# Kernel optimization log

Measured on AMD Instinct MI355X. Metric: run time of the kernel, lower is better.

The kernel has to match this reference:

```python
import jax, jax.numpy as jnp
import numpy as np

DIM = 1024
HEADS = 16
DIM_HEAD = 64
INNER = HEADS * DIM_HEAD  # 1024
EPS = 1e-5


def setup_inputs() -> dict:
    key = jax.random.key(0)
    ks = jax.random.split(key, 8)
    B, N = 4, 2048
    s = 0.02
    return {
        "query": jax.random.normal(ks[0], (B, N, DIM), jnp.float32),
        "key_": jax.random.normal(ks[1], (B, N, DIM), jnp.float32),
        "value": jax.random.normal(ks[2], (B, N, DIM), jnp.float32),
        "Wq": jax.random.normal(ks[3], (DIM, INNER), jnp.float32) * s,
        "Wk": jax.random.normal(ks[4], (DIM, INNER), jnp.float32) * s,
        "Wv": jax.random.normal(ks[5], (DIM, INNER), jnp.float32) * s,
        "Wo": jax.random.normal(ks[6], (INNER, DIM), jnp.float32) * s,
        "bo": jnp.zeros((DIM,), jnp.float32),
        "gamma": jnp.ones((DIM,), jnp.float32),
        "beta": jnp.zeros((DIM,), jnp.float32),
    }


def reference(query, key_, value, Wq, Wk, Wv, Wo, bo, gamma, beta):
    B, N, _ = query.shape
    scale = DIM_HEAD ** (-0.5)
    # project and split heads: [B, H, N, Dh]
    q = (query @ Wq).reshape(B, N, HEADS, DIM_HEAD).transpose(0, 2, 1, 3)
    k = (key_ @ Wk).reshape(B, N, HEADS, DIM_HEAD).transpose(0, 2, 1, 3)
    v = (value @ Wv).reshape(B, N, HEADS, DIM_HEAD).transpose(0, 2, 1, 3)
    dots = jnp.einsum("bhnd,bhmd->bhnm", q, k) * scale  # [B,H,N,N]
    attn = jax.nn.softmax(dots, axis=-1)
    out = jnp.einsum("bhnm,bhmd->bhnd", attn, v)
    out = out.transpose(0, 2, 1, 3).reshape(B, N, INNER)
    out = out @ Wo + bo  # dropout p=0.0 is identity
    # LayerNorm over last dim
    mu = out.mean(-1, keepdims=True)
    var = ((out - mu) ** 2).mean(-1, keepdims=True)
    normed = (out - mu) * jax.lax.rsqrt(var + EPS) * gamma + beta
    return normed + query
```

## Files before the change

### kernel.cpp

```cpp
#include <hip/hip_runtime.h>
#include <stdint.h>

#define K_DIM 1024
#define B_SZ 4
#define N_SEQ 2048
#define HEADS 16
#define DH 64
#define M_TOT (B_SZ * N_SEQ)

typedef __bf16 bf16x8 __attribute__((ext_vector_type(8)));
typedef __bf16 bf16x4 __attribute__((ext_vector_type(4)));
typedef float f32x4 __attribute__((ext_vector_type(4)));

typedef const uint32_t __attribute__((address_space(1))) gas_u32;
typedef uint32_t __attribute__((address_space(3))) las_u32;

__device__ __forceinline__ uint16_t f2bf(float f) {
  uint32_t u = __float_as_uint(f);
  u += 0x7FFFu + ((u >> 16) & 1u);
  return (uint16_t)(u >> 16);
}

__device__ __forceinline__ void gld_lds16(const uint16_t* g, uint16_t* lds) {
  __builtin_amdgcn_global_load_lds((gas_u32*)g, (las_u32*)lds, 16, 0, 0);
}

__global__ __launch_bounds__(256) void conv_bf16_k(const float* __restrict__ src,
                                                   uint16_t* __restrict__ dst, int n4) {
  int i = blockIdx.x * blockDim.x + threadIdx.x;
  if (i < n4) {
    float4 v = ((const float4*)src)[i];
    ushort4 o;
    o.x = f2bf(v.x); o.y = f2bf(v.y); o.z = f2bf(v.z); o.w = f2bf(v.w);
    ((ushort4*)dst)[i] = o;
  }
}

__global__ __launch_bounds__(256) void transpose_conv(const float* __restrict__ src,
                                                      uint16_t* __restrict__ dst) {
  __shared__ float tile[32][33];
  const int tx = threadIdx.x, ty = threadIdx.y;
  const int bx = blockIdx.x * 32, by = blockIdx.y * 32;
#pragma unroll
  for (int i = 0; i < 32; i += 8)
    tile[ty + i][tx] = src[(size_t)(by + ty + i) * 1024 + bx + tx];
  __syncthreads();
#pragma unroll
  for (int i = 0; i < 32; i += 8)
    dst[(size_t)(bx + ty + i) * 1024 + by + tx] = f2bf(tile[tx][ty + i]);
}

template <int MODE>
__global__ __launch_bounds__(256, 2) void gemm_bf16(const uint16_t* __restrict__ A,
                                                    const uint16_t* __restrict__ BT,
                                                    void* __restrict__ Cout,
                                                    const float* __restrict__ bias) {
  __shared__ __align__(16) uint16_t As[128 * 32];
  __shared__ __align__(16) uint16_t Bs[128 * 32];
  const int tid = threadIdx.x;
  const int wave = tid >> 6, lane = tid & 63;
  const int g = lane >> 4, c16 = lane & 15;
  const int m0 = blockIdx.y * 128, n0 = blockIdx.x * 128;
  const int wr = wave >> 1, wc = wave & 1;

  const f32x4 fzero = {0.f, 0.f, 0.f, 0.f};
  f32x4 acc[4][4];
#pragma unroll
  for (int i = 0; i < 4; ++i)
#pragma unroll
    for (int j = 0; j < 4; ++j) acc[i][j] = fzero;

  const int srow = wave * 32 + (lane >> 2);
  const int scol = (lane & 3) * 8;
  const uint16_t* ag0 = A + (size_t)(m0 + srow) * K_DIM + scol;
  const uint16_t* ag1 = A + (size_t)(m0 + srow + 16) * K_DIM + scol;
  const uint16_t* bg0 = BT + (size_t)(n0 + srow) * K_DIM + scol;
  const uint16_t* bg1 = BT + (size_t)(n0 + srow + 16) * K_DIM + scol;
  uint16_t* la0 = &As[(wave * 32) * 32];
  uint16_t* la1 = &As[(wave * 32 + 16) * 32];
  uint16_t* lb0 = &Bs[(wave * 32) * 32];
  uint16_t* lb1 = &Bs[(wave * 32 + 16) * 32];

  for (int kt = 0; kt < K_DIM / 32; ++kt) {
    __syncthreads();
    gld_lds16(ag0 + kt * 32, la0);
    gld_lds16(ag1 + kt * 32, la1);
    gld_lds16(bg0 + kt * 32, lb0);
    gld_lds16(bg1 + kt * 32, lb1);
    __syncthreads();
    bf16x8 avec[4], bvec[4];
#pragma unroll
    for (int i = 0; i < 4; ++i)
      avec[i] = *(const bf16x8*)&As[(wr * 64 + i * 16 + c16) * 32 + g * 8];
#pragma unroll
    for (int j = 0; j < 4; ++j)
      bvec[j] = *(const bf16x8*)&Bs[(wc * 64 + j * 16 + c16) * 32 + g * 8];
#pragma unroll
    for (int i = 0; i < 4; ++i)
#pragma unroll
      for (int j = 0; j < 4; ++j)
        acc[i][j] = __builtin_amdgcn_mfma_f32_16x16x32_bf16(avec[i], bvec[j], acc[i][j], 0, 0, 0);
  }

#pragma unroll
  for (int i = 0; i < 4; ++i) {
#pragma unroll
    for (int j = 0; j < 4; ++j) {
      const int col = n0 + wc * 64 + j * 16 + c16;
      if (MODE == 2) {
        const int h = col >> 6, d = col & 63;
        const int row0 = m0 + wr * 64 + i * 16 + g * 4;
        const int b = row0 >> 11, n = row0 & 2047;
        ushort4 o;
        o.x = f2bf(acc[i][j][0]); o.y = f2bf(acc[i][j][1]);
        o.z = f2bf(acc[i][j][2]); o.w = f2bf(acc[i][j][3]);
        *(ushort4*)&((uint16_t*)Cout)[(((size_t)(b * HEADS + h)) * DH + d) * N_SEQ + n] = o;
      } else {
#pragma unroll
        for (int r = 0; r < 4; ++r) {
          const int row = m0 + wr * 64 + i * 16 + g * 4 + r;
          if (MODE == 0) {
            const int b = row >> 11, n = row & 2047;
            const int h = col >> 6, d = col & 63;
            ((uint16_t*)Cout)[(((size_t)(b * HEADS + h)) * N_SEQ + n) * DH + d] = f2bf(acc[i][j][r]);
          } else {
            ((float*)Cout)[(size_t)row * 1024 + col] = acc[i][j][r] + bias[col];
          }
        }
      }
    }
  }
}

__global__ __launch_bounds__(256, 2) void attention_k(const uint16_t* __restrict__ qm,
                                                      const uint16_t* __restrict__ km,
                                                      const uint16_t* __restrict__ vtm,
                                                      uint16_t* __restrict__ om) {
  __shared__ __align__(16) uint16_t Ks[64 * 72];
  __shared__ __align__(16) uint16_t Vs[64 * 72];
  __shared__ __align__(16) uint16_t Pt[4][64 * 88];
  const int tid = threadIdx.x;
  const int wave = tid >> 6, lane = tid & 63;
  const int g = lane >> 4, c16 = lane & 15;
  const int bh = blockIdx.y, b = bh >> 4, h = bh & 15;
  const int q0 = blockIdx.x * 256 + wave * 64;

  const uint16_t* qbase = qm + (size_t)bh * N_SEQ * DH;
  const uint16_t* kbase = km + (size_t)bh * N_SEQ * DH;
  const uint16_t* vbase = vtm + (size_t)bh * DH * N_SEQ;

  bf16x8 qf[4][2];
#pragma unroll
  for (int qc = 0; qc < 4; ++qc) {
    const uint16_t* qp = qbase + (size_t)(q0 + qc * 16 + c16) * DH + g * 8;
    qf[qc][0] = *(const bf16x8*)qp;
    qf[qc][1] = *(const bf16x8*)(qp + 32);
  }

  const f32x4 fz = {0.f, 0.f, 0.f, 0.f};
  f32x4 oacc[4][4];
#pragma unroll
  for (int qc = 0; qc < 4; ++qc)
#pragma unroll
    for (int jt = 0; jt < 4; ++jt) oacc[qc][jt] = fz;
  float l[4] = {0.f, 0.f, 0.f, 0.f};

  const float CE = 0.1803368801f;
  uint16_t* ptw = Pt[wave];

  for (int t = 0; t < N_SEQ / 64; ++t) {
    __syncthreads();
#pragma unroll
    for (int p = 0; p < 2; ++p) {
      const int e = (p * 256 + tid) * 8;
      *(uint4*)&Ks[(e >> 6) * 72 + (e & 63)] = *(const uint4*)&kbase[(size_t)t * 4096 + e];
      const int c = p * 256 + tid;
      const int vr = c >> 3, vc = (c & 7) * 8;
      *(uint4*)&Vs[vr * 72 + vc] = *(const uint4*)&vbase[(size_t)vr * N_SEQ + t * 64 + vc];
    }
    __syncthreads();

#pragma unroll
    for (int kt = 0; kt < 4; ++kt) {
      bf16x8 kf0 = *(const bf16x8*)&Ks[(kt * 16 + c16) * 72 + g * 8];
      bf16x8 kf1 = *(const bf16x8*)&Ks[(kt * 16 + c16) * 72 + 32 + g * 8];
#pragma unroll
      for (int qc = 0; qc < 4; ++qc) {
        f32x4 z = fz;
        z = __builtin_amdgcn_mfma_f32_16x16x32_bf16(kf0, qf[qc][0], z, 0, 0, 0);
        z = __builtin_amdgcn_mfma_f32_16x16x32_bf16(kf1, qf[qc][1], z, 0, 0, 0);
        const float p0 = __builtin_amdgcn_exp2f(z[0] * CE);
        const float p1 = __builtin_amdgcn_exp2f(z[1] * CE);
        const float p2 = __builtin_amdgcn_exp2f(z[2] * CE);
        const float p3 = __builtin_amdgcn_exp2f(z[3] * CE);
        l[qc] += (p0 + p1) + (p2 + p3);
        bf16x4 pk;
        pk[0] = (__bf16)p0; pk[1] = (__bf16)p1; pk[2] = (__bf16)p2; pk[3] = (__bf16)p3;
        *(bf16x4*)&ptw[(qc * 16 + c16) * 88 + kt * 16 + g * 4] = pk;
      }
    }

#pragma unroll
    for (int kc = 0; kc < 2; ++kc) {
      bf16x8 pa[4];
#pragma unroll
      for (int qc = 0; qc < 4; ++qc)
        pa[qc] = *(const bf16x8*)&ptw[(qc * 16 + c16) * 88 + kc * 32 + g * 8];
#pragma unroll
      for (int jt = 0; jt < 4; ++jt) {
        bf16x8 vb = *(const bf16x8*)&Vs[(jt * 16 + c16) * 72 + kc * 32 + g * 8];
#pragma unroll
        for (int qc = 0; qc < 4; ++qc)
          oacc[qc][jt] = __builtin_amdgcn_mfma_f32_16x16x32_bf16(pa[qc], vb, oacc[qc][jt], 0, 0, 0);
      }
    }
  }

#pragma unroll
  for (int qc = 0; qc < 4; ++qc) {
    l[qc] += __shfl_xor(l[qc], 16);
    l[qc] += __shfl_xor(l[qc], 32);
  }

#pragma unroll
  for (int qc = 0; qc < 4; ++qc) {
#pragma unroll
    for (int r = 0; r < 4; ++r) {
      const float lr = __shfl(l[qc], g * 4 + r, 16);
      const float inv = 1.f / lr;
      const int row = q0 + qc * 16 + g * 4 + r;
      const size_t base = ((size_t)b * N_SEQ + row) * 1024 + h * 64;
#pragma unroll
      for (int jt = 0; jt < 4; ++jt)
        om[base + jt * 16 + c16] = f2bf(oacc[qc][jt][r] * inv);
    }
  }
}

__global__ __launch_bounds__(256) void ln_res_k(const float* __restrict__ proj,
                                                const float* __restrict__ query,
                                                const float* __restrict__ gamma,
                                                const float* __restrict__ beta,
                                                float* __restrict__ out) {
  const int row = blockIdx.x;
  const int tid = threadIdx.x;
  const size_t base = (size_t)row * 1024 + tid * 4;
  float4 v = *(const float4*)(proj + base);
  float s = v.x + v.y + v.z + v.w;
  float s2 = v.x * v.x + v.y * v.y + v.z * v.z + v.w * v.w;
#pragma unroll
  for (int off = 1; off < 64; off <<= 1) {
    s += __shfl_xor(s, off);
    s2 += __shfl_xor(s2, off);
  }
  __shared__ float red[8];
  const int wave = tid >> 6, lane = tid & 63;
  if (lane == 0) { red[wave] = s; red[4 + wave] = s2; }
  __syncthreads();
  s = red[0] + red[1] + red[2] + red[3];
  s2 = red[4] + red[5] + red[6] + red[7];
  const float mu = s * (1.f / 1024.f);
  const float var = fmaxf(s2 * (1.f / 1024.f) - mu * mu, 0.f);
  const float rstd = rsqrtf(var + 1e-5f);
  float4 gq = *(const float4*)(gamma + tid * 4);
  float4 bq = *(const float4*)(beta + tid * 4);
  float4 qq = *(const float4*)(query + base);
  float4 o;
  o.x = (v.x - mu) * rstd * gq.x + bq.x + qq.x;
  o.y = (v.y - mu) * rstd * gq.y + bq.y + qq.y;
  o.z = (v.z - mu) * rstd * gq.z + bq.z + qq.z;
  o.w = (v.w - mu) * rstd * gq.w + bq.w + qq.w;
  *(float4*)(out + base) = o;
}

extern "C" void kernel_launch(void* const* d_in, const int* in_sizes, int n_in,
                              void* d_out, int out_size, void* d_ws, size_t ws_size,
                              hipStream_t stream) {
  (void)in_sizes; (void)n_in; (void)out_size; (void)ws_size;
  const float* query = (const float*)d_in[0];
  const float* key_ = (const float*)d_in[1];
  const float* value = (const float*)d_in[2];
  const float* Wq = (const float*)d_in[3];
  const float* Wk = (const float*)d_in[4];
  const float* Wv = (const float*)d_in[5];
  const float* Wo = (const float*)d_in[6];
  const float* bo = (const float*)d_in[7];
  const float* gamma = (const float*)d_in[8];
  const float* beta = (const float*)d_in[9];
  float* out = (float*)d_out;

  const size_t NELEM = (size_t)M_TOT * 1024;
  uint16_t* wsp = (uint16_t*)d_ws;
  uint16_t* WqT = wsp;
  uint16_t* WkT = WqT + 1024 * 1024;
  uint16_t* WvT = WkT + 1024 * 1024;
  uint16_t* WoT = WvT + 1024 * 1024;
  uint16_t* xq = WoT + 1024 * 1024;
  uint16_t* xk = xq + NELEM;
  uint16_t* xv = xk + NELEM;
  uint16_t* qb = xv + NELEM;
  uint16_t* kb = qb + NELEM;
  uint16_t* vt = kb + NELEM;
  uint16_t* attnO = xq;
  float* proj = (float*)xk;

  const int n4 = (int)(NELEM / 4);
  conv_bf16_k<<<8192, 256, 0, stream>>>(query, xq, n4);
  conv_bf16_k<<<8192, 256, 0, stream>>>(key_, xk, n4);
  conv_bf16_k<<<8192, 256, 0, stream>>>(value, xv, n4);

  dim3 tb(32, 8);
  transpose_conv<<<dim3(32, 32), tb, 0, stream>>>(Wq, WqT);
  transpose_conv<<<dim3(32, 32), tb, 0, stream>>>(Wk, WkT);
  transpose_conv<<<dim3(32, 32), tb, 0, stream>>>(Wv, WvT);
  transpose_conv<<<dim3(32, 32), tb, 0, stream>>>(Wo, WoT);

  dim3 gg(8, 64);
  gemm_bf16<0><<<gg, 256, 0, stream>>>(xq, WqT, qb, nullptr);
  gemm_bf16<0><<<gg, 256, 0, stream>>>(xk, WkT, kb, nullptr);
  gemm_bf16<2><<<gg, 256, 0, stream>>>(xv, WvT, vt, nullptr);

  attention_k<<<dim3(N_SEQ / 256, 64), 256, 0, stream>>>(qb, kb, vt, attnO);

  gemm_bf16<1><<<gg, 256, 0, stream>>>(attnO, WoT, proj, bo);

  ln_res_k<<<8192, 256, 0, stream>>>(proj, query, gamma, beta, out);
}
```

Before: 391.2 us.

## Batch launches, fold softmax scale into Q, swizzle attention LDS, shrink attention tiles

Merges the three input conversions, the four weight transposes and the Q/K projection GEMMs into single launches indexed by blockIdx.y or blockIdx.z. The softmax scale (with the log2e factor) is folded into the Q projection epilogue, which removes a multiply per score in the attention loop. Attention LDS tiles drop their padding in favour of XOR swizzling to avoid bank conflicts. Each wave now handles 32 query rows instead of 64, with launch bounds raised to 4 blocks and twice as many blocks. The trade-off is that each K/V tile loaded into LDS is reused by fewer query rows.

```diff
diff --git a/kernel.cpp b/kernel.cpp
--- a/kernel.cpp
+++ b/kernel.cpp
@@ -15,6 +15,8 @@
 typedef const uint32_t __attribute__((address_space(1))) gas_u32;
 typedef uint32_t __attribute__((address_space(3))) las_u32;
 
+#define CE_SCALE 0.1803368801f
+
 __device__ __forceinline__ uint16_t f2bf(float f) {
   uint32_t u = __float_as_uint(f);
   u += 0x7FFFu + ((u >> 16) & 1u);
@@ -25,8 +27,13 @@
   __builtin_amdgcn_global_load_lds((gas_u32*)g, (las_u32*)lds, 16, 0, 0);
 }
 
-__global__ __launch_bounds__(256) void conv_bf16_k(const float* __restrict__ src,
-                                                   uint16_t* __restrict__ dst, int n4) {
+__global__ __launch_bounds__(256) void conv_bf16_k(const float* __restrict__ s0,
+                                                   const float* __restrict__ s1,
+                                                   const float* __restrict__ s2,
+                                                   uint16_t* __restrict__ dstbase, int n4) {
+  const int z = blockIdx.y;
+  const float* src = (z == 0) ? s0 : (z == 1) ? s1 : s2;
+  uint16_t* dst = dstbase + (size_t)z * M_TOT * K_DIM;
   int i = blockIdx.x * blockDim.x + threadIdx.x;
   if (i < n4) {
     float4 v = ((const float4*)src)[i];
@@ -36,9 +43,15 @@
   }
 }
 
-__global__ __launch_bounds__(256) void transpose_conv(const float* __restrict__ src,
-                                                      uint16_t* __restrict__ dst) {
+__global__ __launch_bounds__(256) void transpose_conv(const float* __restrict__ s0,
+                                                      const float* __restrict__ s1,
+                                                      const float* __restrict__ s2,
+                                                      const float* __restrict__ s3,
+                                                      uint16_t* __restrict__ dstbase) {
   __shared__ float tile[32][33];
+  const int z = blockIdx.z;
+  const float* src = (z == 0) ? s0 : (z == 1) ? s1 : (z == 2) ? s2 : s3;
+  uint16_t* dst = dstbase + (size_t)z * 1024 * 1024;
   const int tx = threadIdx.x, ty = threadIdx.y;
   const int bx = blockIdx.x * 32, by = blockIdx.y * 32;
 #pragma unroll
@@ -62,6 +75,14 @@
   const int g = lane >> 4, c16 = lane & 15;
   const int m0 = blockIdx.y * 128, n0 = blockIdx.x * 128;
   const int wr = wave >> 1, wc = wave & 1;
+  float scale = 1.f;
+  if (MODE == 0) {
+    const int z = blockIdx.z;
+    A += (size_t)z * M_TOT * K_DIM;
+    BT += (size_t)z * 1024 * 1024;
+    Cout = (void*)((uint16_t*)Cout + (size_t)z * M_TOT * K_DIM);
+    scale = (z == 0) ? CE_SCALE : 1.f;
+  }
 
   const f32x4 fzero = {0.f, 0.f, 0.f, 0.f};
   f32x4 acc[4][4];
@@ -122,7 +143,8 @@
           if (MODE == 0) {
             const int b = row >> 11, n = row & 2047;
             const int h = col >> 6, d = col & 63;
-            ((uint16_t*)Cout)[(((size_t)(b * HEADS + h)) * N_SEQ + n) * DH + d] = f2bf(acc[i][j][r]);
+            ((uint16_t*)Cout)[(((size_t)(b * HEADS + h)) * N_SEQ + n) * DH + d] =
+                f2bf(acc[i][j][r] * scale);
           } else {
             ((float*)Cout)[(size_t)row * 1024 + col] = acc[i][j][r] + bias[col];
           }
@@ -132,98 +154,106 @@
   }
 }
 
-__global__ __launch_bounds__(256, 2) void attention_k(const uint16_t* __restrict__ qm,
+__global__ __launch_bounds__(256, 4) void attention_k(const uint16_t* __restrict__ qm,
                                                       const uint16_t* __restrict__ km,
                                                       const uint16_t* __restrict__ vtm,
                                                       uint16_t* __restrict__ om) {
-  __shared__ __align__(16) uint16_t Ks[64 * 72];
-  __shared__ __align__(16) uint16_t Vs[64 * 72];
-  __shared__ __align__(16) uint16_t Pt[4][64 * 88];
+  __shared__ __align__(16) uint16_t Ks[64 * 64];
+  __shared__ __align__(16) uint16_t Vs[64 * 64];
+  __shared__ __align__(16) uint16_t Pt[4][32 * 64];
   const int tid = threadIdx.x;
   const int wave = tid >> 6, lane = tid & 63;
   const int g = lane >> 4, c16 = lane & 15;
   const int bh = blockIdx.y, b = bh >> 4, h = bh & 15;
-  const int q0 = blockIdx.x * 256 + wave * 64;
+  const int q0 = blockIdx.x * 128 + wave * 32;
 
   const uint16_t* qbase = qm + (size_t)bh * N_SEQ * DH;
   const uint16_t* kbase = km + (size_t)bh * N_SEQ * DH;
   const uint16_t* vbase = vtm + (size_t)bh * DH * N_SEQ;
 
-  bf16x8 qf[4][2];
-#pragma unroll
-  for (int qc = 0; qc < 4; ++qc) {
+  bf16x8 qf[2][2];
+#pragma unroll
+  for (int qc = 0; qc < 2; ++qc) {
     const uint16_t* qp = qbase + (size_t)(q0 + qc * 16 + c16) * DH + g * 8;
     qf[qc][0] = *(const bf16x8*)qp;
     qf[qc][1] = *(const bf16x8*)(qp + 32);
   }
 
   const f32x4 fz = {0.f, 0.f, 0.f, 0.f};
-  f32x4 oacc[4][4];
-#pragma unroll
-  for (int qc = 0; qc < 4; ++qc)
+  f32x4 oacc[2][4];
+#pragma unroll
+  for (int qc = 0; qc < 2; ++qc)
 #pragma unroll
     for (int jt = 0; jt < 4; ++jt) oacc[qc][jt] = fz;
-  float l[4] = {0.f, 0.f, 0.f, 0.f};
-
-  const float CE = 0.1803368801f;
+  float l[2] = {0.f, 0.f};
+
   uint16_t* ptw = Pt[wave];
+  const int sw = c16 & 7;
 
   for (int t = 0; t < N_SEQ / 64; ++t) {
     __syncthreads();
 #pragma unroll
     for (int p = 0; p < 2; ++p) {
-      const int e = (p * 256 + tid) * 8;
-      *(uint4*)&Ks[(e >> 6) * 72 + (e & 63)] = *(const uint4*)&kbase[(size_t)t * 4096 + e];
-      const int c = p * 256 + tid;
-      const int vr = c >> 3, vc = (c & 7) * 8;
-      *(uint4*)&Vs[vr * 72 + vc] = *(const uint4*)&vbase[(size_t)vr * N_SEQ + t * 64 + vc];
+      const int idx = p * 256 + tid;
+      {
+        const int e = idx * 8, row = e >> 6, ch = idx & 7;
+        *(uint4*)&Ks[row * 64 + ((ch ^ (row & 7)) << 3)] =
+            *(const uint4*)&kbase[(size_t)t * 4096 + e];
+      }
+      {
+        const int vr = idx >> 3, ch = idx & 7;
+        *(uint4*)&Vs[vr * 64 + ((ch ^ (vr & 7)) << 3)] =
+            *(const uint4*)&vbase[(size_t)vr * N_SEQ + t * 64 + ch * 8];
+      }
     }
     __syncthreads();
 
 #pragma unroll
     for (int kt = 0; kt < 4; ++kt) {
-      bf16x8 kf0 = *(const bf16x8*)&Ks[(kt * 16 + c16) * 72 + g * 8];
-      bf16x8 kf1 = *(const bf16x8*)&Ks[(kt * 16 + c16) * 72 + 32 + g * 8];
-#pragma unroll
-      for (int qc = 0; qc < 4; ++qc) {
+      const int krow = kt * 16 + c16;
+      bf16x8 kf0 = *(const bf16x8*)&Ks[krow * 64 + ((g ^ sw) << 3)];
+      bf16x8 kf1 = *(const bf16x8*)&Ks[krow * 64 + (((4 + g) ^ sw) << 3)];
+#pragma unroll
+      for (int qc = 0; qc < 2; ++qc) {
         f32x4 z = fz;
         z = __builtin_amdgcn_mfma_f32_16x16x32_bf16(kf0, qf[qc][0], z, 0, 0, 0);
         z = __builtin_amdgcn_mfma_f32_16x16x32_bf16(kf1, qf[qc][1], z, 0, 0, 0);
-        const float p0 = __builtin_amdgcn_exp2f(z[0] * CE);
-        const float p1 = __builtin_amdgcn_exp2f(z[1] * CE);
-        const float p2 = __builtin_amdgcn_exp2f(z[2] * CE);
-        const float p3 = __builtin_amdgcn_exp2f(z[3] * CE);
+        const float p0 = __builtin_amdgcn_exp2f(z[0]);
+        const float p1 = __builtin_amdgcn_exp2f(z[1]);
+        const float p2 = __builtin_amdgcn_exp2f(z[2]);
+        const float p3 = __builtin_amdgcn_exp2f(z[3]);
         l[qc] += (p0 + p1) + (p2 + p3);
         bf16x4 pk;
         pk[0] = (__bf16)p0; pk[1] = (__bf16)p1; pk[2] = (__bf16)p2; pk[3] = (__bf16)p3;
-        *(bf16x4*)&ptw[(qc * 16 + c16) * 88 + kt * 16 + g * 4] = pk;
+        *(bf16x4*)&ptw[(qc * 16 + c16) * 64 + (((kt * 2 + (g >> 1)) ^ sw) << 3) + (g & 1) * 4] = pk;
       }
     }
 
 #pragma unroll
     for (int kc = 0; kc < 2; ++kc) {
-      bf16x8 pa[4];
-#pragma unroll
-      for (int qc = 0; qc < 4; ++qc)
-        pa[qc] = *(const bf16x8*)&ptw[(qc * 16 + c16) * 88 + kc * 32 + g * 8];
+      bf16x8 pa[2];
+#pragma unroll
+      for (int qc = 0; qc < 2; ++qc)
+        pa[qc] = *(const bf16x8*)&ptw[(qc * 16 + c16) * 64 + (((kc * 4 + g) ^ sw) << 3)];
 #pragma unroll
       for (int jt = 0; jt < 4; ++jt) {
-        bf16x8 vb = *(const bf16x8*)&Vs[(jt * 16 + c16) * 72 + kc * 32 + g * 8];
-#pragma unroll
-        for (int qc = 0; qc < 4; ++qc)
+        const int vrow = jt * 16 + c16;
+        bf16x8 vb = *(const bf16x8*)&Vs[vrow * 64 + (((kc * 4 + g) ^ sw) << 3)];
+#pragma unroll
+        for (int qc = 0; qc < 2; ++qc)
           oacc[qc][jt] = __builtin_amdgcn_mfma_f32_16x16x32_bf16(pa[qc], vb, oacc[qc][jt], 0, 0, 0);
       }
     }
   }
 
 #pragma unroll
-  for (int qc = 0; qc < 4; ++qc) {
+  for (int qc = 0; qc < 2; ++qc) {
     l[qc] += __shfl_xor(l[qc], 16);
     l[qc] += __shfl_xor(l[qc], 32);
   }
 
 #pragma unroll
-  for (int qc = 0; qc < 4; ++qc) {
+  for (int qc = 0; qc < 2; ++qc) {
 #pragma unroll
     for (int r = 0; r < 4; ++r) {
       const float lr = __shfl(l[qc], g * 4 + r, 16);
@@ -292,37 +322,26 @@
   const size_t NELEM = (size_t)M_TOT * 1024;
   uint16_t* wsp = (uint16_t*)d_ws;
   uint16_t* WqT = wsp;
-  uint16_t* WkT = WqT + 1024 * 1024;
-  uint16_t* WvT = WkT + 1024 * 1024;
-  uint16_t* WoT = WvT + 1024 * 1024;
-  uint16_t* xq = WoT + 1024 * 1024;
-  uint16_t* xk = xq + NELEM;
-  uint16_t* xv = xk + NELEM;
-  uint16_t* qb = xv + NELEM;
-  uint16_t* kb = qb + NELEM;
-  uint16_t* vt = kb + NELEM;
+  uint16_t* WvT = WqT + 2 * 1024 * 1024;
+  uint16_t* WoT = WqT + 3 * 1024 * 1024;
+  uint16_t* xq = WqT + 4 * 1024 * 1024;
+  uint16_t* xv = xq + 2 * NELEM;
+  uint16_t* qb = xq + 3 * NELEM;
+  uint16_t* vt = qb + 2 * NELEM;
   uint16_t* attnO = xq;
-  float* proj = (float*)xk;
+  float* proj = (float*)(xq + NELEM);
 
   const int n4 = (int)(NELEM / 4);
-  conv_bf16_k<<<8192, 256, 0, stream>>>(query, xq, n4);
-  conv_bf16_k<<<8192, 256, 0, stream>>>(key_, xk, n4);
-  conv_bf16_k<<<8192, 256, 0, stream>>>(value, xv, n4);
-
-  dim3 tb(32, 8);
-  transpose_conv<<<dim3(32, 32), tb, 0, stream>>>(Wq, WqT);
-  transpose_conv<<<dim3(32, 32), tb, 0, stream>>>(Wk, WkT);
-  transpose_conv<<<dim3(32, 32), tb, 0, stream>>>(Wv, WvT);
-  transpose_conv<<<dim3(32, 32), tb, 0, stream>>>(Wo, WoT);
-
-  dim3 gg(8, 64);
-  gemm_bf16<0><<<gg, 256, 0, stream>>>(xq, WqT, qb, nullptr);
-  gemm_bf16<0><<<gg, 256, 0, stream>>>(xk, WkT, kb, nullptr);
-  gemm_bf16<2><<<gg, 256, 0, stream>>>(xv, WvT, vt, nullptr);
-
-  attention_k<<<dim3(N_SEQ / 256, 64), 256, 0, stream>>>(qb, kb, vt, attnO);
-
-  gemm_bf16<1><<<gg, 256, 0, stream>>>(attnO, WoT, proj, bo);
+  conv_bf16_k<<<dim3(8192, 3), 256, 0, stream>>>(query, key_, value, xq, n4);
+
+  transpose_conv<<<dim3(32, 32, 4), dim3(32, 8), 0, stream>>>(Wq, Wk, Wv, Wo, WqT);
+
+  gemm_bf16<0><<<dim3(8, 64, 2), 256, 0, stream>>>(xq, WqT, qb, nullptr);
+  gemm_bf16<2><<<dim3(8, 64), 256, 0, stream>>>(xv, WvT, vt, nullptr);
+
+  attention_k<<<dim3(N_SEQ / 128, 64), 256, 0, stream>>>(qb, qb + NELEM, vt, attnO);
+
+  gemm_bf16<1><<<dim3(8, 64), 256, 0, stream>>>(attnO, WoT, proj, bo);
 
   ln_res_k<<<8192, 256, 0, stream>>>(proj, query, gamma, beta, out);
 }
```

Result: faster. 374.2 us (-4.4%).
